# Performance work log

Measured on AMD Instinct MI355X. Metric: run time of the kernel, lower is better.

Reference implementation:

```python
import jax, jax.numpy as jnp
from jax import lax
import numpy as np

B, T, F, H, C = 32, 1000, 161, 512, 62

def setup_inputs() -> dict:
    key = jax.random.key(0)
    ks = jax.random.split(key, 12)
    s = lambda *sh: 1.0 / np.sqrt(sh[0])
    inp = {
        'x': jax.random.normal(ks[0], (B, T, F), jnp.float32),
        'seq_lens': jax.random.randint(ks[1], (B,), T // 2, T + 1, jnp.int32),
        'w1': jax.random.normal(ks[2], (F, H), jnp.float32) * s(F),
        'b1': jnp.zeros((H,), jnp.float32),
        'w2': jax.random.normal(ks[3], (H, H), jnp.float32) * s(H),
        'b2': jnp.zeros((H,), jnp.float32),
        'wg_f': jax.random.normal(ks[4], (2 * H, 2 * H), jnp.float32) * s(2 * H),
        'bg_f': jnp.ones((2 * H,), jnp.float32),  # TF GRU gate bias init = 1.0
        'wc_f': jax.random.normal(ks[5], (2 * H, H), jnp.float32) * s(2 * H),
        'bc_f': jnp.zeros((H,), jnp.float32),
        'wg_b': jax.random.normal(ks[6], (2 * H, 2 * H), jnp.float32) * s(2 * H),
        'bg_b': jnp.ones((2 * H,), jnp.float32),
        'wc_b': jax.random.normal(ks[7], (2 * H, H), jnp.float32) * s(2 * H),
        'bc_b': jnp.zeros((H,), jnp.float32),
        'wf': jax.random.normal(ks[8], (2 * H, C), jnp.float32) * s(2 * H),
        'bf': jnp.zeros((C,), jnp.float32),
    }
    return inp


def _reverse_sequence(x, lens):
    # mimic tf.reverse_sequence along time axis 1
    t = jnp.arange(x.shape[1])  # [T]
    idx = jnp.where(t[None, :] < lens[:, None], lens[:, None] - 1 - t[None, :], t[None, :])  # [B,T]
    return jnp.take_along_axis(x, idx[:, :, None], axis=1)


def _run_gru(x, lens, wg, bg, wc, bc):
    # x: [B,T,H] -> outputs [B,T,H]; zero output and frozen state past lens (dynamic_rnn semantics)
    xT = jnp.swapaxes(x, 0, 1)  # [T,B,H]
    h0 = jnp.zeros((x.shape[0], bc.shape[0]), x.dtype)

    def step(h, inp):
        xt, t = inp
        ru = jax.nn.sigmoid(jnp.concatenate([xt, h], axis=-1) @ wg + bg)
        r, u = jnp.split(ru, 2, axis=-1)
        c = jnp.tanh(jnp.concatenate([xt, r * h], axis=-1) @ wc + bc)
        hn = u * h + (1.0 - u) * c
        mask = (t < lens)[:, None]
        h_new = jnp.where(mask, hn, h)
        out = jnp.where(mask, hn, jnp.zeros_like(hn))
        return h_new, out

    _, outs = lax.scan(step, h0, (xT, jnp.arange(x.shape[1])))
    return jnp.swapaxes(outs, 0, 1)


def reference(x, seq_lens, w1, b1, w2, b2, wg_f, bg_f, wc_f, bc_f, wg_b, bg_b, wc_b, bc_b, wf, bf):
    h = jax.nn.relu(x @ w1 + b1)
    h = jax.nn.relu(h @ w2 + b2)  # [B,T,H]
    out_f = _run_gru(h, seq_lens, wg_f, bg_f, wc_f, bc_f)
    h_rev = _reverse_sequence(h, seq_lens)
    out_b = _reverse_sequence(_run_gru(h_rev, seq_lens, wg_b, bg_b, wc_b, bc_b), seq_lens)
    scores = jnp.concatenate([out_f, out_b], axis=2)  # [B,T,2H]
    logits = scores @ wf + bf  # [B,T,C]
    return logits
```

## Files before the change

kernel.cpp:

```cpp
#include <hip/hip_runtime.h>
#include <hip/hip_bf16.h>
#include <cstdint>

#define B_  32
#define T_  1000
#define F_  161
#define H_  512
#define C_  62
#define BT_ 32000
#define TC  200
#define NCH 5
#define MCH (B_ * TC)
#define NB_ 32

typedef __bf16 bf16x8 __attribute__((ext_vector_type(8)));
typedef float  f32x4  __attribute__((ext_vector_type(4)));
typedef unsigned short us8 __attribute__((ext_vector_type(8)));

__device__ __forceinline__ float b2f(unsigned short s) {
    union { unsigned int i; float f; } v; v.i = (unsigned int)s << 16; return v.f;
}
__device__ __forceinline__ unsigned short f2b(float f) {
    unsigned int u = __float_as_uint(f);
    unsigned int r = u + 0x7fffu + ((u >> 16) & 1u);
    return (unsigned short)(r >> 16);
}


__global__ __launch_bounds__(256) void cvt_x_pad(const float* __restrict__ x,
                                                 unsigned short* __restrict__ xb) {
    int idx = blockIdx.x * 256 + threadIdx.x;
    if (idx >= BT_ * 192) return;
    int r = idx / 192, k = idx - r * 192;
    float v = (k < F_) ? x[(size_t)r * F_ + k] : 0.f;
    xb[idx] = f2b(v);
}

__global__ __launch_bounds__(256) void transpose_cvt(const float* __restrict__ src,
                                                     unsigned short* __restrict__ dst,
                                                     int K, int N, int k0, int KP, int NP) {
    int idx = blockIdx.x * 256 + threadIdx.x;
    if (idx >= NP * KP) return;
    int n = idx / KP, k = idx - n * KP;
    float v = (k < K && n < N) ? src[(size_t)(k0 + k) * N + n] : 0.f;
    dst[idx] = f2b(v);
}

__global__ __launch_bounds__(256) void biascat(const float* __restrict__ bg_f,
                                               const float* __restrict__ bc_f,
                                               const float* __restrict__ bg_b,
                                               const float* __restrict__ bc_b,
                                               float* __restrict__ bcat) {
    int idx = blockIdx.x * 256 + threadIdx.x;
    if (idx >= 2 * 1536) return;
    int d = idx / 1536, c = idx - d * 1536;
    const float* bg = d ? bg_b : bg_f;
    const float* bc = d ? bc_b : bc_f;
    bcat[idx] = (c < 1024) ? bg[c] : bc[c - 1024];
}


#define BM 128
#define BN 64
#define BK 64

template<bool RELU, int OMODE, bool AMAP>
__global__ __launch_bounds__(256) void gemm_bf16(const unsigned short* __restrict__ A,
                                                 const unsigned short* __restrict__ BT,
                                                 const float* __restrict__ bias,
                                                 void* __restrict__ Out,
                                                 int K, int Nreal, int t0) {
    __shared__ __align__(16) unsigned short As[BM * BK];
    __shared__ __align__(16) unsigned short Bs[BN * BK];
    const int tid  = threadIdx.x;
    const int lane = tid & 63;
    const int w    = tid >> 6;
    const int wm   = w & 1, wn = w >> 1;
    const int l15  = lane & 15, l4 = lane >> 4;
    const int m0   = blockIdx.x * BM;
    const int n0   = blockIdx.y * BN;

    const int ar = tid >> 1, ac = (tid & 1) * 32;
    const int br = tid >> 2, bc = (tid & 3) * 16;

    size_t arow;
    {
        int r = m0 + ar;
        if (AMAP) { int rb = r / TC; int rt = r - rb * TC; arow = (size_t)rb * T_ + t0 + rt; }
        else      arow = (size_t)r;
    }

    f32x4 acc[4][2] = {};

    for (int kt = 0; kt < K; kt += BK) {
        if (kt) __syncthreads();
        {
            const unsigned short* ga = A + arow * K + kt + ac;
            us8* la = (us8*)(As + ar * BK + ac);
            #pragma unroll
            for (int j = 0; j < 4; ++j) la[j] = *(const us8*)(ga + 8 * j);
            const unsigned short* gb = BT + (size_t)(n0 + br) * K + kt + bc;
            us8* lb = (us8*)(Bs + br * BK + bc);
            #pragma unroll
            for (int j = 0; j < 2; ++j) lb[j] = *(const us8*)(gb + 8 * j);
        }
        __syncthreads();
        #pragma unroll
        for (int kk = 0; kk < BK; kk += 32) {
            bf16x8 af[4], bfr[2];
            #pragma unroll
            for (int m = 0; m < 4; ++m)
                af[m] = *(const bf16x8*)(As + (wm * 64 + m * 16 + l15) * BK + kk + l4 * 8);
            #pragma unroll
            for (int n = 0; n < 2; ++n)
                bfr[n] = *(const bf16x8*)(Bs + (wn * 32 + n * 16 + l15) * BK + kk + l4 * 8);
            #pragma unroll
            for (int m = 0; m < 4; ++m)
                #pragma unroll
                for (int n = 0; n < 2; ++n)
                    acc[m][n] = __builtin_amdgcn_mfma_f32_16x16x32_bf16(af[m], bfr[n], acc[m][n], 0, 0, 0);
        }
    }

    const int rbase = m0 + wm * 64;
    const int cb    = n0 + wn * 32;
    #pragma unroll
    for (int m = 0; m < 4; ++m) {
        #pragma unroll
        for (int n = 0; n < 2; ++n) {
            int gc = cb + n * 16 + l15;
            if (gc < Nreal) {
                float bv = bias ? bias[gc] : 0.f;
                int gr0 = rbase + m * 16 + l4 * 4;
                #pragma unroll
                for (int r = 0; r < 4; ++r) {
                    float v = acc[m][n][r] + bv;
                    if (RELU) v = fmaxf(v, 0.f);
                    int gr = gr0 + r;
                    if (OMODE == 0) {
                        ((unsigned short*)Out)[(size_t)gr * Nreal + gc] = f2b(v);
                    } else {
                        int rb = gr / TC; int rt = gr - rb * TC;
                        size_t orow = (size_t)rb * T_ + t0 + rt;
                        ((float*)Out)[orow * Nreal + gc] += v;
                    }
                }
            }
        }
    }
}


__global__ __launch_bounds__(512) void gru_persist(const unsigned short* __restrict__ wh_f,
                                                   const unsigned short* __restrict__ wh_b,
                                                   const unsigned short* __restrict__ Xf,
                                                   const unsigned short* __restrict__ Xb,
                                                   const int* __restrict__ seq_lens,
                                                   float* __restrict__ hf32_glob,
                                                   unsigned int* __restrict__ hb_glob,
                                                   unsigned int* __restrict__ rh_glob,
                                                   unsigned int* __restrict__ flags,
                                                   unsigned short* __restrict__ of,
                                                   unsigned short* __restrict__ ob,
                                                   int t0f, int t0b, int base, int init) {
    __shared__ __align__(16) unsigned short WG[64 * 512];
    __shared__ __align__(16) unsigned short WC[32 * 512];
    __shared__ __align__(16) unsigned short STG[32 * 512];
    __shared__ __align__(16) unsigned short XGs[32 * 64];
    __shared__ __align__(16) unsigned short XCs[32 * 32];
    __shared__ float USH[32][33];
    __shared__ float HOWN[32][32];
    __shared__ int Ls[32];

    const int bid = blockIdx.x;
    const int dir = bid >> 4;
    const int g   = bid & 15;
    const int tid = threadIdx.x;
    const int lane = tid & 63;
    const int w   = tid >> 6;
    const int l15 = lane & 15, l4 = lane >> 4;

    const unsigned short* wh = dir ? wh_b : wh_f;
    const unsigned short* X  = dir ? Xb : Xf;
    unsigned short* out      = dir ? ob : of;
    const int t0 = dir ? t0b : t0f;
    float*        hf32 = hf32_glob + (size_t)dir * 32 * 512;
    unsigned int* hb32 = hb_glob   + (size_t)dir * 32 * 256;
    unsigned int* rh32 = rh_glob   + (size_t)dir * 32 * 256;
    unsigned int* flg  = flags + dir * 256;
    unsigned int* myflag = flg + g * 16;

    for (int j = tid; j < 4096; j += 512) {
        int col = j >> 6, ck = j & 63;
        int srcc = (col < 32) ? (32 * g + col) : (512 + 32 * g + (col - 32));
        int dstb = col * 1024 + ((ck * 16) ^ ((col & 7) << 4));
        *(us8*)((char*)WG + dstb) = *(const us8*)(wh + (size_t)srcc * 512 + ck * 8);
    }
    for (int j = tid; j < 2048; j += 512) {
        int col = j >> 6, ck = j & 63;
        int dstb = col * 1024 + ((ck * 16) ^ ((col & 7) << 4));
        *(us8*)((char*)WC + dstb) = *(const us8*)(wh + (size_t)(1024 + 32 * g + col) * 512 + ck * 8);
    }
    if (tid < 32) {
        int L = seq_lens[tid];
        Ls[tid] = L < 0 ? 0 : (L > T_ ? T_ : L);
    }
    for (int j = tid; j < 1024; j += 512) {
        int row = j >> 5, lc = j & 31;
        HOWN[row][lc] = init ? 0.f : hf32[row * 512 + 32 * g + lc];
    }
    {
        int tt0 = dir ? (TC - 1) : 0;
        if (tid < 256) {
            int b = tid >> 3, part = tid & 7;
            int srcc = (part < 4) ? (32 * g + part * 8) : (512 + 32 * g + (part - 4) * 8);
            *(us8*)(XGs + b * 64 + part * 8) =
                *(const us8*)(X + ((size_t)b * TC + tt0) * 1536 + srcc);
        }
    }

    const int mt = w & 1, nt = w >> 1;
    const int mt2 = w & 1, nt2 = (w >> 1) & 1;

    for (int i = 0; i < TC; ++i) {
        const int tt = dir ? (TC - 1 - i) : i;
        const int t  = t0 + tt;

        if (init && i == 0) {
            for (int j = tid; j < 4096; j += 512) {
                *(unsigned long long*)((char*)STG + j * 8) = 0ull;
            }
        } else {
            const unsigned long long* hb64 = (const unsigned long long*)hb32;
            for (int j = tid; j < 4096; j += 512) {
                int row = j >> 7, ck = j & 127;
                unsigned long long v = __hip_atomic_load(hb64 + row * 128 + ck,
                                          __ATOMIC_RELAXED, __HIP_MEMORY_SCOPE_AGENT);
                int dstb = row * 1024 + ((ck * 8) ^ ((row & 7) << 4));
                *(unsigned long long*)((char*)STG + dstb) = v;
            }
        }
        if (tid < 128) {
            int b = tid >> 2, part = tid & 3;
            *(us8*)(XCs + b * 32 + part * 8) =
                *(const us8*)(X + ((size_t)b * TC + tt) * 1536 + 1024 + 32 * g + part * 8);
        }
        __syncthreads();

        f32x4 acc = {};
        {
            const int arow = mt * 16 + l15;
            const int bcol = nt * 16 + l15;
            const int sa = (arow & 7) << 4, sb = (bcol & 7) << 4;
            const char* pa = (const char*)STG + arow * 1024;
            const char* pb = (const char*)WG + bcol * 1024;
            #pragma unroll
            for (int kk = 0; kk < 16; ++kk) {
                int kb = kk * 64 + l4 * 16;
                bf16x8 a  = *(const bf16x8*)(pa + (kb ^ sa));
                bf16x8 bf = *(const bf16x8*)(pb + (kb ^ sb));
                acc = __builtin_amdgcn_mfma_f32_16x16x32_bf16(a, bf, acc, 0, 0, 0);
            }
        }
        {
            const int colL = nt * 16 + l15;
            #pragma unroll
            for (int r = 0; r < 4; ++r) {
                int row = mt * 16 + l4 * 4 + r;
                float s = acc[r] + b2f(XGs[row * 64 + colL]);
                float sg = 1.f / (1.f + __expf(-s));
                if (colL < 32) {
                    int c = 32 * g + colL;
                    unsigned short ho = *(const unsigned short*)((const char*)STG + row * 1024 +
                                            ((c * 2) ^ ((row & 7) << 4)));
                    unsigned int pr = f2b(sg * b2f(ho));
                    unsigned int po = (unsigned int)__shfl_xor((int)pr, 1);
                    if (!(lane & 1))
                        __hip_atomic_store(rh32 + row * 256 + 16 * g + (colL >> 1),
                                           pr | (po << 16),
                                           __ATOMIC_RELAXED, __HIP_MEMORY_SCOPE_AGENT);
                } else {
                    USH[row][colL - 32] = sg;
                }
            }
        }

        {
            unsigned int tgt = (unsigned)(base + 2 * i + 1);
            __syncthreads();
            if (tid == 0)
                __hip_atomic_store(myflag, tgt, __ATOMIC_RELAXED, __HIP_MEMORY_SCOPE_AGENT);
            if (w == 0) {
                const unsigned int* fp = flg + lane * 16;
                for (;;) {
                    unsigned int v = (lane < 16)
                        ? __hip_atomic_load(fp, __ATOMIC_RELAXED, __HIP_MEMORY_SCOPE_AGENT) : tgt;
                    if (__all(v >= tgt)) break;
                    __builtin_amdgcn_s_sleep(1);
                }
            }
            __syncthreads();
        }

        {
            const unsigned long long* rh64 = (const unsigned long long*)rh32;
            for (int j = tid; j < 4096; j += 512) {
                int row = j >> 7, ck = j & 127;
                unsigned long long v = __hip_atomic_load(rh64 + row * 128 + ck,
                                          __ATOMIC_RELAXED, __HIP_MEMORY_SCOPE_AGENT);
                int dstb = row * 1024 + ((ck * 8) ^ ((row & 7) << 4));
                *(unsigned long long*)((char*)STG + dstb) = v;
            }
        }
        __syncthreads();

        if (w < 4) {
            f32x4 acc2 = {};
            const int arow = mt2 * 16 + l15;
            const int bcol = nt2 * 16 + l15;
            const int sa = (arow & 7) << 4, sb = (bcol & 7) << 4;
            const char* pa = (const char*)STG + arow * 1024;
            const char* pb = (const char*)WC + bcol * 1024;
            #pragma unroll
            for (int kk = 0; kk < 16; ++kk) {
                int kb = kk * 64 + l4 * 16;
                bf16x8 a  = *(const bf16x8*)(pa + (kb ^ sa));
                bf16x8 bf = *(const bf16x8*)(pb + (kb ^ sb));
                acc2 = __builtin_amdgcn_mfma_f32_16x16x32_bf16(a, bf, acc2, 0, 0, 0);
            }
            const int colL2 = nt2 * 16 + l15;
            const int col_c = 32 * g + colL2;
            #pragma unroll
            for (int r = 0; r < 4; ++r) {
                int row = mt2 * 16 + l4 * 4 + r;
                float s = acc2[r] + b2f(XCs[row * 32 + colL2]);
                float cv = tanhf(s);
                float uu = USH[row][colL2];
                float ho = HOWN[row][colL2];
                bool act = (t < Ls[row]);
                float hn = act ? (uu * ho + (1.f - uu) * cv) : ho;
                unsigned short hnb = f2b(hn);
                out[((size_t)row * TC + tt) * 512 + col_c] = act ? hnb : (unsigned short)0;
                unsigned int ph = hnb;
                unsigned int po = (unsigned int)__shfl_xor((int)ph, 1);
                if (!(lane & 1))
                    __hip_atomic_store(hb32 + row * 256 + 16 * g + (colL2 >> 1),
                                       ph | (po << 16),
                                       __ATOMIC_RELAXED, __HIP_MEMORY_SCOPE_AGENT);
                HOWN[row][colL2] = hn;
            }
        } else if (i + 1 < TC) {
            int ttn = dir ? (tt - 1) : (tt + 1);
            int jd = tid - 256;
            int b = jd >> 3, part = jd & 7;
            int srcc = (part < 4) ? (32 * g + part * 8) : (512 + 32 * g + (part - 4) * 8);
            *(us8*)(XGs + b * 64 + part * 8) =
                *(const us8*)(X + ((size_t)b * TC + ttn) * 1536 + srcc);
        }

        {
            unsigned int tgt = (unsigned)(base + 2 * i + 2);
            __syncthreads();
            if (tid == 0)
                __hip_atomic_store(myflag, tgt, __ATOMIC_RELAXED, __HIP_MEMORY_SCOPE_AGENT);
            if (w == 0) {
                const unsigned int* fp = flg + lane * 16;
                for (;;) {
                    unsigned int v = (lane < 16)
                        ? __hip_atomic_load(fp, __ATOMIC_RELAXED, __HIP_MEMORY_SCOPE_AGENT) : tgt;
                    if (__all(v >= tgt)) break;
                    __builtin_amdgcn_s_sleep(1);
                }
            }
            __syncthreads();
        }
    }

    for (int j = tid; j < 1024; j += 512) {
        int row = j >> 5, lc = j & 31;
        hf32[row * 512 + 32 * g + lc] = HOWN[row][lc];
    }
}


extern "C" void kernel_launch(void* const* d_in, const int* in_sizes, int n_in,
                              void* d_out, int out_size, void* d_ws, size_t ws_size,
                              hipStream_t stream) {
    (void)in_sizes; (void)n_in; (void)out_size; (void)ws_size;
    const float* x    = (const float*)d_in[0];
    const int*   seq  = (const int*)  d_in[1];
    const float* w1   = (const float*)d_in[2];
    const float* b1   = (const float*)d_in[3];
    const float* w2   = (const float*)d_in[4];
    const float* b2   = (const float*)d_in[5];
    const float* wg_f = (const float*)d_in[6];
    const float* bg_f = (const float*)d_in[7];
    const float* wc_f = (const float*)d_in[8];
    const float* bc_f = (const float*)d_in[9];
    const float* wg_b = (const float*)d_in[10];
    const float* bg_b = (const float*)d_in[11];
    const float* wc_b = (const float*)d_in[12];
    const float* bc_b = (const float*)d_in[13];
    const float* wf   = (const float*)d_in[14];
    const float* bfv  = (const float*)d_in[15];

    char* p = (char*)d_ws;
    auto alloc = [&](size_t bytes) { char* q = p; p += (bytes + 255) & ~(size_t)255; return q; };

    unsigned short* w1T     = (unsigned short*)alloc(512 * 192 * 2);
    unsigned short* w2T     = (unsigned short*)alloc(512 * 512 * 2);
    unsigned short* wx_f    = (unsigned short*)alloc((size_t)1536 * 512 * 2);
    unsigned short* wx_b    = (unsigned short*)alloc((size_t)1536 * 512 * 2);
    unsigned short* wh_f    = (unsigned short*)alloc((size_t)1536 * 512 * 2);
    unsigned short* wh_b    = (unsigned short*)alloc((size_t)1536 * 512 * 2);
    unsigned short* wfT_top = (unsigned short*)alloc(64 * 512 * 2);
    unsigned short* wfT_bot = (unsigned short*)alloc(64 * 512 * 2);
    float*          bcat    = (float*)         alloc(2 * 1536 * 4);

    unsigned short* hB = (unsigned short*)alloc((size_t)BT_ * 512 * 2);

    char* U = alloc((size_t)MCH * 1536 * 2 * 2 + (size_t)MCH * 512 * 2 * 2);
    unsigned short* xb = (unsigned short*)U;
    unsigned short* h1 = (unsigned short*)(U + (size_t)BT_ * 192 * 2);
    unsigned short* Xf = (unsigned short*)U;
    unsigned short* Xb = (unsigned short*)(U + (size_t)MCH * 1536 * 2);
    unsigned short* of = (unsigned short*)(U + (size_t)MCH * 1536 * 2 * 2);
    unsigned short* ob = (unsigned short*)(U + (size_t)MCH * 1536 * 2 * 2 + (size_t)MCH * 512 * 2);

    unsigned int*   flags    = (unsigned int*)alloc(2 * 256 * 4);
    float*          hf32_gl  = (float*)       alloc((size_t)2 * 32 * 512 * 4);
    unsigned int*   hb_gl    = (unsigned int*)alloc((size_t)2 * 32 * 256 * 4);
    unsigned int*   rh_gl    = (unsigned int*)alloc((size_t)2 * 32 * 256 * 4);

    hipMemsetAsync(d_out, 0, (size_t)BT_ * C_ * 4, stream);
    hipMemsetAsync(flags, 0, 2 * 256 * 4, stream);

    transpose_cvt<<<(512 * 192) / 256, 256, 0, stream>>>(w1, w1T, 161, 512, 0, 192, 512);
    transpose_cvt<<<(512 * 512) / 256, 256, 0, stream>>>(w2, w2T, 512, 512, 0, 512, 512);
    transpose_cvt<<<(1024 * 512) / 256, 256, 0, stream>>>(wg_f, wx_f, 512, 1024, 0, 512, 1024);
    transpose_cvt<<<(512 * 512) / 256, 256, 0, stream>>>(wc_f, wx_f + (size_t)1024 * 512, 512, 512, 0, 512, 512);
    transpose_cvt<<<(1024 * 512) / 256, 256, 0, stream>>>(wg_b, wx_b, 512, 1024, 0, 512, 1024);
    transpose_cvt<<<(512 * 512) / 256, 256, 0, stream>>>(wc_b, wx_b + (size_t)1024 * 512, 512, 512, 0, 512, 512);
    transpose_cvt<<<(1024 * 512) / 256, 256, 0, stream>>>(wg_f, wh_f, 512, 1024, 512, 512, 1024);
    transpose_cvt<<<(512 * 512) / 256, 256, 0, stream>>>(wc_f, wh_f + (size_t)1024 * 512, 512, 512, 512, 512, 512);
    transpose_cvt<<<(1024 * 512) / 256, 256, 0, stream>>>(wg_b, wh_b, 512, 1024, 512, 512, 1024);
    transpose_cvt<<<(512 * 512) / 256, 256, 0, stream>>>(wc_b, wh_b + (size_t)1024 * 512, 512, 512, 512, 512, 512);
    transpose_cvt<<<(64 * 512) / 256, 256, 0, stream>>>(wf, wfT_top, 512, 62, 0, 512, 64);
    transpose_cvt<<<(64 * 512) / 256, 256, 0, stream>>>(wf, wfT_bot, 512, 62, 512, 512, 64);
    biascat<<<(2 * 1536 + 255) / 256, 256, 0, stream>>>(bg_f, bc_f, bg_b, bc_b, bcat);

    cvt_x_pad<<<(BT_ * 192 + 255) / 256, 256, 0, stream>>>(x, xb);
    gemm_bf16<true, 0, false><<<dim3(BT_ / BM, 512 / BN), 256, 0, stream>>>(xb, w1T, b1, h1, 192, 512, 0);
    gemm_bf16<true, 0, false><<<dim3(BT_ / BM, 512 / BN), 256, 0, stream>>>(h1, w2T, b2, hB, 512, 512, 0);

    for (int c = 0; c < NCH; ++c) {
        const int t0f = c * TC;
        const int t0b = (NCH - 1 - c) * TC;
        gemm_bf16<false, 0, true><<<dim3(MCH / BM, 1536 / BN), 256, 0, stream>>>(hB, wx_f, bcat,        Xf, 512, 1536, t0f);
        gemm_bf16<false, 0, true><<<dim3(MCH / BM, 1536 / BN), 256, 0, stream>>>(hB, wx_b, bcat + 1536, Xb, 512, 1536, t0b);
        gru_persist<<<NB_, 512, 0, stream>>>(wh_f, wh_b, Xf, Xb, seq, hf32_gl, hb_gl, rh_gl,
                                             flags, of, ob, t0f, t0b, c * 2 * TC, c == 0 ? 1 : 0);
        gemm_bf16<false, 1, false><<<dim3(MCH / BM, 1), 256, 0, stream>>>(of, wfT_top, bfv,     d_out, 512, C_, t0f);
        gemm_bf16<false, 1, false><<<dim3(MCH / BM, 1), 256, 0, stream>>>(ob, wfT_bot, nullptr, d_out, 512, C_, t0b);
    }
}
```

Before: 9.852 ms.

## Pin GRU blocks to one XCD per direction and sync through L2-local buffers

```diff
diff --git a/kernel.cpp b/kernel.cpp
--- a/kernel.cpp
+++ b/kernel.cpp
@@ -11,7 +11,7 @@
 #define TC  200
 #define NCH 5
 #define MCH (B_ * TC)
-#define NB_ 32
+#define FAST_TRIES 64
 
 typedef __bf16 bf16x8 __attribute__((ext_vector_type(8)));
 typedef float  f32x4  __attribute__((ext_vector_type(4)));
@@ -24,6 +24,16 @@
     unsigned int u = __float_as_uint(f);
     unsigned int r = u + 0x7fffu + ((u >> 16) & 1u);
     return (unsigned short)(r >> 16);
+}
+
+__device__ __forceinline__ unsigned int ld_sc0_u32(const unsigned int* p) {
+    unsigned int v;
+    asm volatile("global_load_dword %0, %1, off sc0\n\ts_waitcnt vmcnt(0)"
+                 : "=&v"(v) : "v"(p) : "memory");
+    return v;
+}
+__device__ __forceinline__ void st_sc0_u32(unsigned int* p, unsigned int v) {
+    asm volatile("global_store_dword %0, %1, off sc0" :: "v"(p), "v"(v) : "memory");
 }
 
 
@@ -151,15 +161,72 @@
 }
 
 
+__device__ __forceinline__ void stage_bcast(unsigned short* STG,
+                                            const unsigned int* srcA,
+                                            const unsigned int* srcL,
+                                            int mode, int tid) {
+    if (mode) {
+        const unsigned long long* s64 = (const unsigned long long*)srcA;
+        for (int j = tid; j < 4096; j += 512) {
+            int row = j >> 7, ck = j & 127;
+            unsigned long long v = __hip_atomic_load(s64 + row * 128 + ck,
+                                      __ATOMIC_RELAXED, __HIP_MEMORY_SCOPE_AGENT);
+            int dstb = row * 1024 + ((ck * 8) ^ ((row & 7) << 4));
+            *(unsigned long long*)((char*)STG + dstb) = v;
+        }
+    } else {
+        const int bck = tid & 127;
+        const int br0 = tid >> 7;
+        const unsigned long long* s64 = (const unsigned long long*)srcL;
+        const unsigned long long* a0 = s64 + (br0 +  0) * 128 + bck;
+        const unsigned long long* a1 = s64 + (br0 +  4) * 128 + bck;
+        const unsigned long long* a2 = s64 + (br0 +  8) * 128 + bck;
+        const unsigned long long* a3 = s64 + (br0 + 12) * 128 + bck;
+        const unsigned long long* a4 = s64 + (br0 + 16) * 128 + bck;
+        const unsigned long long* a5 = s64 + (br0 + 20) * 128 + bck;
+        const unsigned long long* a6 = s64 + (br0 + 24) * 128 + bck;
+        const unsigned long long* a7 = s64 + (br0 + 28) * 128 + bck;
+        unsigned long long v0, v1, v2, v3, v4, v5, v6, v7;
+        asm volatile(
+            "global_load_dwordx2 %0, %8, off sc0\n\t"
+            "global_load_dwordx2 %1, %9, off sc0\n\t"
+            "global_load_dwordx2 %2, %10, off sc0\n\t"
+            "global_load_dwordx2 %3, %11, off sc0\n\t"
+            "global_load_dwordx2 %4, %12, off sc0\n\t"
+            "global_load_dwordx2 %5, %13, off sc0\n\t"
+            "global_load_dwordx2 %6, %14, off sc0\n\t"
+            "global_load_dwordx2 %7, %15, off sc0\n\t"
+            "s_waitcnt vmcnt(0)"
+            : "=&v"(v0), "=&v"(v1), "=&v"(v2), "=&v"(v3),
+              "=&v"(v4), "=&v"(v5), "=&v"(v6), "=&v"(v7)
+            : "v"(a0), "v"(a1), "v"(a2), "v"(a3),
+              "v"(a4), "v"(a5), "v"(a6), "v"(a7)
+            : "memory");
+        const int swz = bck * 8;
+        *(unsigned long long*)((char*)STG + (br0 +  0) * 1024 + (swz ^ (((br0 +  0) & 7) << 4))) = v0;
+        *(unsigned long long*)((char*)STG + (br0 +  4) * 1024 + (swz ^ (((br0 +  4) & 7) << 4))) = v1;
+        *(unsigned long long*)((char*)STG + (br0 +  8) * 1024 + (swz ^ (((br0 +  8) & 7) << 4))) = v2;
+        *(unsigned long long*)((char*)STG + (br0 + 12) * 1024 + (swz ^ (((br0 + 12) & 7) << 4))) = v3;
+        *(unsigned long long*)((char*)STG + (br0 + 16) * 1024 + (swz ^ (((br0 + 16) & 7) << 4))) = v4;
+        *(unsigned long long*)((char*)STG + (br0 + 20) * 1024 + (swz ^ (((br0 + 20) & 7) << 4))) = v5;
+        *(unsigned long long*)((char*)STG + (br0 + 24) * 1024 + (swz ^ (((br0 + 24) & 7) << 4))) = v6;
+        *(unsigned long long*)((char*)STG + (br0 + 28) * 1024 + (swz ^ (((br0 + 28) & 7) << 4))) = v7;
+    }
+}
+
 __global__ __launch_bounds__(512) void gru_persist(const unsigned short* __restrict__ wh_f,
                                                    const unsigned short* __restrict__ wh_b,
                                                    const unsigned short* __restrict__ Xf,
                                                    const unsigned short* __restrict__ Xb,
                                                    const int* __restrict__ seq_lens,
                                                    float* __restrict__ hf32_glob,
-                                                   unsigned int* __restrict__ hb_glob,
-                                                   unsigned int* __restrict__ rh_glob,
-                                                   unsigned int* __restrict__ flags,
+                                                   unsigned int* __restrict__ hbA_g,
+                                                   unsigned int* __restrict__ hbL_g,
+                                                   unsigned int* __restrict__ rhA_g,
+                                                   unsigned int* __restrict__ rhL_g,
+                                                   unsigned int* __restrict__ flagsA,
+                                                   unsigned int* __restrict__ flagsL,
+                                                   int* __restrict__ claim,
                                                    unsigned short* __restrict__ of,
                                                    unsigned short* __restrict__ ob,
                                                    int t0f, int t0b, int base, int init) {
@@ -171,11 +238,29 @@
     __shared__ float USH[32][33];
     __shared__ float HOWN[32][32];
     __shared__ int Ls[32];
-
-    const int bid = blockIdx.x;
-    const int dir = bid >> 4;
-    const int g   = bid & 15;
+    __shared__ int role_sh;
+    __shared__ int mode_sh;
+
     const int tid = threadIdx.x;
+
+    if (tid == 0) {
+        unsigned int xcd;
+        asm volatile("s_getreg_b32 %0, hwreg(HW_REG_XCC_ID)" : "=s"(xcd));
+        xcd &= 7u;
+        int r = -1;
+        if (xcd < 2u) {
+            int s = atomicAdd(&claim[xcd], 1);
+            if (s < 16) r = (int)(xcd * 16u) + s;
+        }
+        role_sh = r;
+        mode_sh = 0;
+    }
+    __syncthreads();
+    const int role = role_sh;
+    if (role < 0) return;
+    const int dir = role >> 4;
+    const int g   = role & 15;
+
     const int lane = tid & 63;
     const int w   = tid >> 6;
     const int l15 = lane & 15, l4 = lane >> 4;
@@ -185,10 +270,14 @@
     unsigned short* out      = dir ? ob : of;
     const int t0 = dir ? t0b : t0f;
     float*        hf32 = hf32_glob + (size_t)dir * 32 * 512;
-    unsigned int* hb32 = hb_glob   + (size_t)dir * 32 * 256;
-    unsigned int* rh32 = rh_glob   + (size_t)dir * 32 * 256;
-    unsigned int* flg  = flags + dir * 256;
-    unsigned int* myflag = flg + g * 16;
+    unsigned int* hbA  = hbA_g + (size_t)dir * 32 * 256;
+    unsigned int* hbL  = hbL_g + (size_t)dir * 32 * 256;
+    unsigned int* rhA  = rhA_g + (size_t)dir * 32 * 256;
+    unsigned int* rhL  = rhL_g + (size_t)dir * 32 * 256;
+    unsigned int* flgA = flagsA + dir * 256;
+    unsigned int* flgL = flagsL + dir * 256;
+    unsigned int* myflagA = flgA + g * 16;
+    unsigned int* myflagL = flgL + g * 16;
 
     for (int j = tid; j < 4096; j += 512) {
         int col = j >> 6, ck = j & 63;
@@ -227,18 +316,10 @@
         const int t  = t0 + tt;
 
         if (init && i == 0) {
-            for (int j = tid; j < 4096; j += 512) {
+            for (int j = tid; j < 4096; j += 512)
                 *(unsigned long long*)((char*)STG + j * 8) = 0ull;
-            }
         } else {
-            const unsigned long long* hb64 = (const unsigned long long*)hb32;
-            for (int j = tid; j < 4096; j += 512) {
-                int row = j >> 7, ck = j & 127;
-                unsigned long long v = __hip_atomic_load(hb64 + row * 128 + ck,
-                                          __ATOMIC_RELAXED, __HIP_MEMORY_SCOPE_AGENT);
-                int dstb = row * 1024 + ((ck * 8) ^ ((row & 7) << 4));
-                *(unsigned long long*)((char*)STG + dstb) = v;
-            }
+            stage_bcast(STG, hbA, hbL, mode_sh, tid);
         }
         if (tid < 128) {
             int b = tid >> 2, part = tid & 3;
@@ -251,14 +332,14 @@
         {
             const int arow = mt * 16 + l15;
             const int bcol = nt * 16 + l15;
-            const int sa = (arow & 7) << 4, sb = (bcol & 7) << 4;
+            const int sa = (arow & 7) << 4, sb2 = (bcol & 7) << 4;
             const char* pa = (const char*)STG + arow * 1024;
             const char* pb = (const char*)WG + bcol * 1024;
             #pragma unroll
             for (int kk = 0; kk < 16; ++kk) {
                 int kb = kk * 64 + l4 * 16;
                 bf16x8 a  = *(const bf16x8*)(pa + (kb ^ sa));
-                bf16x8 bf = *(const bf16x8*)(pb + (kb ^ sb));
+                bf16x8 bf = *(const bf16x8*)(pb + (kb ^ sb2));
                 acc = __builtin_amdgcn_mfma_f32_16x16x32_bf16(a, bf, acc, 0, 0, 0);
             }
         }
@@ -275,10 +356,13 @@
                                             ((c * 2) ^ ((row & 7) << 4)));
                     unsigned int pr = f2b(sg * b2f(ho));
                     unsigned int po = (unsigned int)__shfl_xor((int)pr, 1);
-                    if (!(lane & 1))
-                        __hip_atomic_store(rh32 + row * 256 + 16 * g + (colL >> 1),
-                                           pr | (po << 16),
+                    if (!(lane & 1)) {
+                        unsigned int word = pr | (po << 16);
+                        int off = row * 256 + 16 * g + (colL >> 1);
+                        __hip_atomic_store(rhA + off, word,
                                            __ATOMIC_RELAXED, __HIP_MEMORY_SCOPE_AGENT);
+                        st_sc0_u32(rhL + off, word);
+                    }
                 } else {
                     USH[row][colL - 32] = sg;
                 }
@@ -288,44 +372,44 @@
         {
             unsigned int tgt = (unsigned)(base + 2 * i + 1);
             __syncthreads();
-            if (tid == 0)
-                __hip_atomic_store(myflag, tgt, __ATOMIC_RELAXED, __HIP_MEMORY_SCOPE_AGENT);
+            if (tid == 0) {
+                __hip_atomic_store(myflagA, tgt, __ATOMIC_RELAXED, __HIP_MEMORY_SCOPE_AGENT);
+                st_sc0_u32(myflagL, tgt);
+            }
             if (w == 0) {
-                const unsigned int* fp = flg + lane * 16;
+                bool ua = (mode_sh != 0);
+                int tries = 0;
+                const unsigned int* fpA = flgA + lane * 16;
+                const unsigned int* fpL = flgL + lane * 16;
                 for (;;) {
-                    unsigned int v = (lane < 16)
-                        ? __hip_atomic_load(fp, __ATOMIC_RELAXED, __HIP_MEMORY_SCOPE_AGENT) : tgt;
+                    unsigned int v = tgt;
+                    if (lane < 16)
+                        v = ua ? __hip_atomic_load(fpA, __ATOMIC_RELAXED, __HIP_MEMORY_SCOPE_AGENT)
+                               : ld_sc0_u32(fpL);
                     if (__all(v >= tgt)) break;
+                    if (!ua && ++tries >= FAST_TRIES) ua = true;
                     __builtin_amdgcn_s_sleep(1);
                 }
+                if (ua && lane == 0) mode_sh = 1;
             }
             __syncthreads();
         }
 
-        {
-            const unsigned long long* rh64 = (const unsigned long long*)rh32;
-            for (int j = tid; j < 4096; j += 512) {
-                int row = j >> 7, ck = j & 127;
-                unsigned long long v = __hip_atomic_load(rh64 + row * 128 + ck,
-                                          __ATOMIC_RELAXED, __HIP_MEMORY_SCOPE_AGENT);
-                int dstb = row * 1024 + ((ck * 8) ^ ((row & 7) << 4));
-                *(unsigned long long*)((char*)STG + dstb) = v;
-            }
-        }
+        stage_bcast(STG, rhA, rhL, mode_sh, tid);
         __syncthreads();
 
         if (w < 4) {
             f32x4 acc2 = {};
             const int arow = mt2 * 16 + l15;
             const int bcol = nt2 * 16 + l15;
-            const int sa = (arow & 7) << 4, sb = (bcol & 7) << 4;
+            const int sa = (arow & 7) << 4, sb2 = (bcol & 7) << 4;
             const char* pa = (const char*)STG + arow * 1024;
             const char* pb = (const char*)WC + bcol * 1024;
             #pragma unroll
             for (int kk = 0; kk < 16; ++kk) {
                 int kb = kk * 64 + l4 * 16;
                 bf16x8 a  = *(const bf16x8*)(pa + (kb ^ sa));
-                bf16x8 bf = *(const bf16x8*)(pb + (kb ^ sb));
+                bf16x8 bf = *(const bf16x8*)(pb + (kb ^ sb2));
                 acc2 = __builtin_amdgcn_mfma_f32_16x16x32_bf16(a, bf, acc2, 0, 0, 0);
             }
             const int colL2 = nt2 * 16 + l15;
@@ -343,10 +427,13 @@
                 out[((size_t)row * TC + tt) * 512 + col_c] = act ? hnb : (unsigned short)0;
                 unsigned int ph = hnb;
                 unsigned int po = (unsigned int)__shfl_xor((int)ph, 1);
-                if (!(lane & 1))
-                    __hip_atomic_store(hb32 + row * 256 + 16 * g + (colL2 >> 1),
-                                       ph | (po << 16),
+                if (!(lane & 1)) {
+                    unsigned int word = ph | (po << 16);
+                    int off = row * 256 + 16 * g + (colL2 >> 1);
+                    __hip_atomic_store(hbA + off, word,
                                        __ATOMIC_RELAXED, __HIP_MEMORY_SCOPE_AGENT);
+                    st_sc0_u32(hbL + off, word);
+                }
                 HOWN[row][colL2] = hn;
             }
         } else if (i + 1 < TC) {
@@ -361,16 +448,25 @@
         {
             unsigned int tgt = (unsigned)(base + 2 * i + 2);
             __syncthreads();
-            if (tid == 0)
-                __hip_atomic_store(myflag, tgt, __ATOMIC_RELAXED, __HIP_MEMORY_SCOPE_AGENT);
+            if (tid == 0) {
+                __hip_atomic_store(myflagA, tgt, __ATOMIC_RELAXED, __HIP_MEMORY_SCOPE_AGENT);
+                st_sc0_u32(myflagL, tgt);
+            }
             if (w == 0) {
-                const unsigned int* fp = flg + lane * 16;
+                bool ua = (mode_sh != 0);
+                int tries = 0;
+                const unsigned int* fpA = flgA + lane * 16;
+                const unsigned int* fpL = flgL + lane * 16;
                 for (;;) {
-                    unsigned int v = (lane < 16)
-                        ? __hip_atomic_load(fp, __ATOMIC_RELAXED, __HIP_MEMORY_SCOPE_AGENT) : tgt;
+                    unsigned int v = tgt;
+                    if (lane < 16)
+                        v = ua ? __hip_atomic_load(fpA, __ATOMIC_RELAXED, __HIP_MEMORY_SCOPE_AGENT)
+                               : ld_sc0_u32(fpL);
                     if (__all(v >= tgt)) break;
+                    if (!ua && ++tries >= FAST_TRIES) ua = true;
                     __builtin_amdgcn_s_sleep(1);
                 }
+                if (ua && lane == 0) mode_sh = 1;
             }
             __syncthreads();
         }
@@ -427,13 +523,17 @@
     unsigned short* of = (unsigned short*)(U + (size_t)MCH * 1536 * 2 * 2);
     unsigned short* ob = (unsigned short*)(U + (size_t)MCH * 1536 * 2 * 2 + (size_t)MCH * 512 * 2);
 
-    unsigned int*   flags    = (unsigned int*)alloc(2 * 256 * 4);
+    unsigned int*   flagsA   = (unsigned int*)alloc(2 * 256 * 4);
+    unsigned int*   flagsL   = (unsigned int*)alloc(2 * 256 * 4);
+    int*            claim    = (int*)         alloc(256);
     float*          hf32_gl  = (float*)       alloc((size_t)2 * 32 * 512 * 4);
-    unsigned int*   hb_gl    = (unsigned int*)alloc((size_t)2 * 32 * 256 * 4);
-    unsigned int*   rh_gl    = (unsigned int*)alloc((size_t)2 * 32 * 256 * 4);
+    unsigned int*   hbA_gl   = (unsigned int*)alloc((size_t)2 * 32 * 256 * 4);
+    unsigned int*   hbL_gl   = (unsigned int*)alloc((size_t)2 * 32 * 256 * 4);
+    unsigned int*   rhA_gl   = (unsigned int*)alloc((size_t)2 * 32 * 256 * 4);
+    unsigned int*   rhL_gl   = (unsigned int*)alloc((size_t)2 * 32 * 256 * 4);
 
     hipMemsetAsync(d_out, 0, (size_t)BT_ * C_ * 4, stream);
-    hipMemsetAsync(flags, 0, 2 * 256 * 4, stream);
+    hipMemsetAsync(flagsA, 0, 2 * 256 * 4 + 2 * 256 * 4 + 256, stream);
 
     transpose_cvt<<<(512 * 192) / 256, 256, 0, stream>>>(w1, w1T, 161, 512, 0, 192, 512);
     transpose_cvt<<<(512 * 512) / 256, 256, 0, stream>>>(w2, w2T, 512, 512, 0, 512, 512);
@@ -458,8 +558,10 @@
         const int t0b = (NCH - 1 - c) * TC;
         gemm_bf16<false, 0, true><<<dim3(MCH / BM, 1536 / BN), 256, 0, stream>>>(hB, wx_f, bcat,        Xf, 512, 1536, t0f);
         gemm_bf16<false, 0, true><<<dim3(MCH / BM, 1536 / BN), 256, 0, stream>>>(hB, wx_b, bcat + 1536, Xb, 512, 1536, t0b);
-        gru_persist<<<NB_, 512, 0, stream>>>(wh_f, wh_b, Xf, Xb, seq, hf32_gl, hb_gl, rh_gl,
-                                             flags, of, ob, t0f, t0b, c * 2 * TC, c == 0 ? 1 : 0);
+        gru_persist<<<256, 512, 0, stream>>>(wh_f, wh_b, Xf, Xb, seq, hf32_gl,
+                                             hbA_gl, hbL_gl, rhA_gl, rhL_gl,
+                                             flagsA, flagsL, claim + 2 * c, of, ob,
+                                             t0f, t0b, c * 2 * TC, c == 0 ? 1 : 0);
         gemm_bf16<false, 1, false><<<dim3(MCH / BM, 1), 256, 0, stream>>>(of, wfT_top, bfv,     d_out, 512, C_, t0f);
         gemm_bf16<false, 1, false><<<dim3(MCH / BM, 1), 256, 0, stream>>>(ob, wfT_bot, nullptr, d_out, 512, C_, t0b);
     }
```

After: 9.283 ms. 5.8% less time.

## Pin GRU blocks per direction to one XCD and use per-peer dataflow flags

Applied to the files above, without the earlier changes.

```diff
diff --git a/kernel.cpp b/kernel.cpp
--- a/kernel.cpp
+++ b/kernel.cpp
@@ -11,7 +11,7 @@
 #define TC  200
 #define NCH 5
 #define MCH (B_ * TC)
-#define NB_ 32
+#define ESC_TRIES (1 << 14)
 
 typedef __bf16 bf16x8 __attribute__((ext_vector_type(8)));
 typedef float  f32x4  __attribute__((ext_vector_type(4)));
@@ -151,15 +151,44 @@
 }
 
 
+__device__ __forceinline__ void wait_flag(const unsigned int* f, unsigned int tgt) {
+    int tries = 0;
+    while (__hip_atomic_load(f, __ATOMIC_RELAXED, __HIP_MEMORY_SCOPE_AGENT) < tgt) {
+        if (++tries >= ESC_TRIES) break;
+        __builtin_amdgcn_s_sleep(1);
+    }
+    asm volatile("" ::: "memory");
+}
+
+__device__ __forceinline__ void stage_peer(unsigned short* STG, const unsigned int* src,
+                                           int q, int lane) {
+    const unsigned long long* s64 = (const unsigned long long*)src;
+    int row = lane >> 1, half = lane & 1;
+    const unsigned long long* a = s64 + row * 128 + 8 * q + 4 * half;
+    unsigned long long d0 = __hip_atomic_load(a + 0, __ATOMIC_RELAXED, __HIP_MEMORY_SCOPE_AGENT);
+    unsigned long long d1 = __hip_atomic_load(a + 1, __ATOMIC_RELAXED, __HIP_MEMORY_SCOPE_AGENT);
+    unsigned long long d2 = __hip_atomic_load(a + 2, __ATOMIC_RELAXED, __HIP_MEMORY_SCOPE_AGENT);
+    unsigned long long d3 = __hip_atomic_load(a + 3, __ATOMIC_RELAXED, __HIP_MEMORY_SCOPE_AGENT);
+    int bb  = 64 * q + 32 * half;
+    int swz = (row & 7) << 4;
+    char* rp = (char*)STG + row * 1024;
+    *(unsigned long long*)(rp + ((bb +  0) ^ swz)) = d0;
+    *(unsigned long long*)(rp + ((bb +  8) ^ swz)) = d1;
+    *(unsigned long long*)(rp + ((bb + 16) ^ swz)) = d2;
+    *(unsigned long long*)(rp + ((bb + 24) ^ swz)) = d3;
+}
+
 __global__ __launch_bounds__(512) void gru_persist(const unsigned short* __restrict__ wh_f,
                                                    const unsigned short* __restrict__ wh_b,
                                                    const unsigned short* __restrict__ Xf,
                                                    const unsigned short* __restrict__ Xb,
                                                    const int* __restrict__ seq_lens,
                                                    float* __restrict__ hf32_glob,
-                                                   unsigned int* __restrict__ hb_glob,
-                                                   unsigned int* __restrict__ rh_glob,
-                                                   unsigned int* __restrict__ flags,
+                                                   unsigned int* __restrict__ hb_g,
+                                                   unsigned int* __restrict__ rh_g,
+                                                   unsigned int* __restrict__ fH_g,
+                                                   unsigned int* __restrict__ fR_g,
+                                                   int* __restrict__ claim,
                                                    unsigned short* __restrict__ of,
                                                    unsigned short* __restrict__ ob,
                                                    int t0f, int t0b, int base, int init) {
@@ -171,11 +200,27 @@
     __shared__ float USH[32][33];
     __shared__ float HOWN[32][32];
     __shared__ int Ls[32];
-
-    const int bid = blockIdx.x;
-    const int dir = bid >> 4;
-    const int g   = bid & 15;
+    __shared__ int role_sh;
+
     const int tid = threadIdx.x;
+
+    if (tid == 0) {
+        unsigned int xcd;
+        asm volatile("s_getreg_b32 %0, hwreg(HW_REG_XCC_ID)" : "=s"(xcd));
+        xcd &= 7u;
+        int r = -1;
+        if (xcd < 2u) {
+            int s = atomicAdd(&claim[xcd], 1);
+            if (s < 16) r = (int)(xcd * 16u) + s;
+        }
+        role_sh = r;
+    }
+    __syncthreads();
+    const int role = role_sh;
+    if (role < 0) return;
+    const int dir = role >> 4;
+    const int g   = role & 15;
+
     const int lane = tid & 63;
     const int w   = tid >> 6;
     const int l15 = lane & 15, l4 = lane >> 4;
@@ -185,10 +230,12 @@
     unsigned short* out      = dir ? ob : of;
     const int t0 = dir ? t0b : t0f;
     float*        hf32 = hf32_glob + (size_t)dir * 32 * 512;
-    unsigned int* hb32 = hb_glob   + (size_t)dir * 32 * 256;
-    unsigned int* rh32 = rh_glob   + (size_t)dir * 32 * 256;
-    unsigned int* flg  = flags + dir * 256;
-    unsigned int* myflag = flg + g * 16;
+    unsigned int* hb0 = hb_g + (size_t)dir * 2 * 8192;
+    unsigned int* rh0 = rh_g + (size_t)dir * 2 * 8192;
+    unsigned int* fH  = fH_g + dir * 256;
+    unsigned int* fR  = fR_g + dir * 256;
+    unsigned int* myfH = fH + g * 16;
+    unsigned int* myfR = fR + g * 16;
 
     for (int j = tid; j < 4096; j += 512) {
         int col = j >> 6, ck = j & 63;
@@ -225,19 +272,18 @@
     for (int i = 0; i < TC; ++i) {
         const int tt = dir ? (TC - 1 - i) : i;
         const int t  = t0 + tt;
+        const unsigned int s = (unsigned)(base + i);
 
         if (init && i == 0) {
-            for (int j = tid; j < 4096; j += 512) {
+            for (int j = tid; j < 4096; j += 512)
                 *(unsigned long long*)((char*)STG + j * 8) = 0ull;
-            }
         } else {
-            const unsigned long long* hb64 = (const unsigned long long*)hb32;
-            for (int j = tid; j < 4096; j += 512) {
-                int row = j >> 7, ck = j & 127;
-                unsigned long long v = __hip_atomic_load(hb64 + row * 128 + ck,
-                                          __ATOMIC_RELAXED, __HIP_MEMORY_SCOPE_AGENT);
-                int dstb = row * 1024 + ((ck * 8) ^ ((row & 7) << 4));
-                *(unsigned long long*)((char*)STG + dstb) = v;
+            const unsigned int* hbs = hb0 + ((s - 1) & 1) * 8192;
+            #pragma unroll
+            for (int k = 0; k < 2; ++k) {
+                int q = 2 * w + k;
+                wait_flag(fH + q * 16, s);
+                stage_peer(STG, hbs, q, lane);
             }
         }
         if (tid < 128) {
@@ -251,24 +297,25 @@
         {
             const int arow = mt * 16 + l15;
             const int bcol = nt * 16 + l15;
-            const int sa = (arow & 7) << 4, sb = (bcol & 7) << 4;
+            const int sa = (arow & 7) << 4, sb2 = (bcol & 7) << 4;
             const char* pa = (const char*)STG + arow * 1024;
             const char* pb = (const char*)WG + bcol * 1024;
             #pragma unroll
             for (int kk = 0; kk < 16; ++kk) {
                 int kb = kk * 64 + l4 * 16;
                 bf16x8 a  = *(const bf16x8*)(pa + (kb ^ sa));
-                bf16x8 bf = *(const bf16x8*)(pb + (kb ^ sb));
+                bf16x8 bf = *(const bf16x8*)(pb + (kb ^ sb2));
                 acc = __builtin_amdgcn_mfma_f32_16x16x32_bf16(a, bf, acc, 0, 0, 0);
             }
         }
         {
+            unsigned int* rhs = rh0 + (s & 1) * 8192;
             const int colL = nt * 16 + l15;
             #pragma unroll
             for (int r = 0; r < 4; ++r) {
                 int row = mt * 16 + l4 * 4 + r;
-                float s = acc[r] + b2f(XGs[row * 64 + colL]);
-                float sg = 1.f / (1.f + __expf(-s));
+                float sv = acc[r] + b2f(XGs[row * 64 + colL]);
+                float sg = 1.f / (1.f + __expf(-sv));
                 if (colL < 32) {
                     int c = 32 * g + colL;
                     unsigned short ho = *(const unsigned short*)((const char*)STG + row * 1024 +
@@ -276,7 +323,7 @@
                     unsigned int pr = f2b(sg * b2f(ho));
                     unsigned int po = (unsigned int)__shfl_xor((int)pr, 1);
                     if (!(lane & 1))
-                        __hip_atomic_store(rh32 + row * 256 + 16 * g + (colL >> 1),
+                        __hip_atomic_store(rhs + row * 256 + 16 * g + (colL >> 1),
                                            pr | (po << 16),
                                            __ATOMIC_RELAXED, __HIP_MEMORY_SCOPE_AGENT);
                 } else {
@@ -284,32 +331,17 @@
                 }
             }
         }
+        __syncthreads();
+        if (tid == 0)
+            __hip_atomic_store(myfR, s + 1, __ATOMIC_RELAXED, __HIP_MEMORY_SCOPE_AGENT);
 
         {
-            unsigned int tgt = (unsigned)(base + 2 * i + 1);
-            __syncthreads();
-            if (tid == 0)
-                __hip_atomic_store(myflag, tgt, __ATOMIC_RELAXED, __HIP_MEMORY_SCOPE_AGENT);
-            if (w == 0) {
-                const unsigned int* fp = flg + lane * 16;
-                for (;;) {
-                    unsigned int v = (lane < 16)
-                        ? __hip_atomic_load(fp, __ATOMIC_RELAXED, __HIP_MEMORY_SCOPE_AGENT) : tgt;
-                    if (__all(v >= tgt)) break;
-                    __builtin_amdgcn_s_sleep(1);
-                }
-            }
-            __syncthreads();
-        }
-
-        {
-            const unsigned long long* rh64 = (const unsigned long long*)rh32;
-            for (int j = tid; j < 4096; j += 512) {
-                int row = j >> 7, ck = j & 127;
-                unsigned long long v = __hip_atomic_load(rh64 + row * 128 + ck,
-                                          __ATOMIC_RELAXED, __HIP_MEMORY_SCOPE_AGENT);
-                int dstb = row * 1024 + ((ck * 8) ^ ((row & 7) << 4));
-                *(unsigned long long*)((char*)STG + dstb) = v;
+            const unsigned int* rhs = rh0 + (s & 1) * 8192;
+            #pragma unroll
+            for (int k = 0; k < 2; ++k) {
+                int q = 2 * w + k;
+                wait_flag(fR + q * 16, s + 1);
+                stage_peer(STG, rhs, q, lane);
             }
         }
         __syncthreads();
@@ -318,23 +350,24 @@
             f32x4 acc2 = {};
             const int arow = mt2 * 16 + l15;
             const int bcol = nt2 * 16 + l15;
-            const int sa = (arow & 7) << 4, sb = (bcol & 7) << 4;
+            const int sa = (arow & 7) << 4, sb2 = (bcol & 7) << 4;
             const char* pa = (const char*)STG + arow * 1024;
             const char* pb = (const char*)WC + bcol * 1024;
             #pragma unroll
             for (int kk = 0; kk < 16; ++kk) {
                 int kb = kk * 64 + l4 * 16;
                 bf16x8 a  = *(const bf16x8*)(pa + (kb ^ sa));
-                bf16x8 bf = *(const bf16x8*)(pb + (kb ^ sb));
+                bf16x8 bf = *(const bf16x8*)(pb + (kb ^ sb2));
                 acc2 = __builtin_amdgcn_mfma_f32_16x16x32_bf16(a, bf, acc2, 0, 0, 0);
             }
+            unsigned int* hbs = hb0 + (s & 1) * 8192;
             const int colL2 = nt2 * 16 + l15;
             const int col_c = 32 * g + colL2;
             #pragma unroll
             for (int r = 0; r < 4; ++r) {
                 int row = mt2 * 16 + l4 * 4 + r;
-                float s = acc2[r] + b2f(XCs[row * 32 + colL2]);
-                float cv = tanhf(s);
+                float sv = acc2[r] + b2f(XCs[row * 32 + colL2]);
+                float cv = tanhf(sv);
                 float uu = USH[row][colL2];
                 float ho = HOWN[row][colL2];
                 bool act = (t < Ls[row]);
@@ -344,7 +377,7 @@
                 unsigned int ph = hnb;
                 unsigned int po = (unsigned int)__shfl_xor((int)ph, 1);
                 if (!(lane & 1))
-                    __hip_atomic_store(hb32 + row * 256 + 16 * g + (colL2 >> 1),
+                    __hip_atomic_store(hbs + row * 256 + 16 * g + (colL2 >> 1),
                                        ph | (po << 16),
                                        __ATOMIC_RELAXED, __HIP_MEMORY_SCOPE_AGENT);
                 HOWN[row][colL2] = hn;
@@ -357,23 +390,9 @@
             *(us8*)(XGs + b * 64 + part * 8) =
                 *(const us8*)(X + ((size_t)b * TC + ttn) * 1536 + srcc);
         }
-
-        {
-            unsigned int tgt = (unsigned)(base + 2 * i + 2);
-            __syncthreads();
-            if (tid == 0)
-                __hip_atomic_store(myflag, tgt, __ATOMIC_RELAXED, __HIP_MEMORY_SCOPE_AGENT);
-            if (w == 0) {
-                const unsigned int* fp = flg + lane * 16;
-                for (;;) {
-                    unsigned int v = (lane < 16)
-                        ? __hip_atomic_load(fp, __ATOMIC_RELAXED, __HIP_MEMORY_SCOPE_AGENT) : tgt;
-                    if (__all(v >= tgt)) break;
-                    __builtin_amdgcn_s_sleep(1);
-                }
-            }
-            __syncthreads();
-        }
+        __syncthreads();
+        if (tid == 0)
+            __hip_atomic_store(myfH, s + 1, __ATOMIC_RELAXED, __HIP_MEMORY_SCOPE_AGENT);
     }
 
     for (int j = tid; j < 1024; j += 512) {
@@ -427,13 +446,15 @@
     unsigned short* of = (unsigned short*)(U + (size_t)MCH * 1536 * 2 * 2);
     unsigned short* ob = (unsigned short*)(U + (size_t)MCH * 1536 * 2 * 2 + (size_t)MCH * 512 * 2);
 
-    unsigned int*   flags    = (unsigned int*)alloc(2 * 256 * 4);
+    unsigned int*   fH_gl    = (unsigned int*)alloc(2 * 256 * 4);
+    unsigned int*   fR_gl    = (unsigned int*)alloc(2 * 256 * 4);
+    int*            claim    = (int*)         alloc(256);
     float*          hf32_gl  = (float*)       alloc((size_t)2 * 32 * 512 * 4);
-    unsigned int*   hb_gl    = (unsigned int*)alloc((size_t)2 * 32 * 256 * 4);
-    unsigned int*   rh_gl    = (unsigned int*)alloc((size_t)2 * 32 * 256 * 4);
+    unsigned int*   hb_gl    = (unsigned int*)alloc((size_t)2 * 2 * 8192 * 4);
+    unsigned int*   rh_gl    = (unsigned int*)alloc((size_t)2 * 2 * 8192 * 4);
 
     hipMemsetAsync(d_out, 0, (size_t)BT_ * C_ * 4, stream);
-    hipMemsetAsync(flags, 0, 2 * 256 * 4, stream);
+    hipMemsetAsync(fH_gl, 0, 2 * 256 * 4 + 2 * 256 * 4 + 256, stream);
 
     transpose_cvt<<<(512 * 192) / 256, 256, 0, stream>>>(w1, w1T, 161, 512, 0, 192, 512);
     transpose_cvt<<<(512 * 512) / 256, 256, 0, stream>>>(w2, w2T, 512, 512, 0, 512, 512);
@@ -458,8 +479,9 @@
         const int t0b = (NCH - 1 - c) * TC;
         gemm_bf16<false, 0, true><<<dim3(MCH / BM, 1536 / BN), 256, 0, stream>>>(hB, wx_f, bcat,        Xf, 512, 1536, t0f);
         gemm_bf16<false, 0, true><<<dim3(MCH / BM, 1536 / BN), 256, 0, stream>>>(hB, wx_b, bcat + 1536, Xb, 512, 1536, t0b);
-        gru_persist<<<NB_, 512, 0, stream>>>(wh_f, wh_b, Xf, Xb, seq, hf32_gl, hb_gl, rh_gl,
-                                             flags, of, ob, t0f, t0b, c * 2 * TC, c == 0 ? 1 : 0);
+        gru_persist<<<256, 512, 0, stream>>>(wh_f, wh_b, Xf, Xb, seq, hf32_gl,
+                                             hb_gl, rh_gl, fH_gl, fR_gl, claim + 2 * c,
+                                             of, ob, t0f, t0b, c * TC, c == 0 ? 1 : 0);
         gemm_bf16<false, 1, false><<<dim3(MCH / BM, 1), 256, 0, stream>>>(of, wfT_top, bfv,     d_out, 512, C_, t0f);
         gemm_bf16<false, 1, false><<<dim3(MCH / BM, 1), 256, 0, stream>>>(ob, wfT_bot, nullptr, d_out, 512, C_, t0b);
     }
```

New measurement: 7.963 ms, median of 2. -19.2%, faster.
